# Optimization experiments

Hardware: AMD Instinct MI355X
Metric: run time of the kernel (lower is better)

## Reference

```python
import jax, jax.numpy as jnp
import numpy as np

IN, HID, RANK, B = 2048, 2048, 512, 8192


def setup_inputs() -> dict:
    key = jax.random.key(0)
    ks = jax.random.split(key, 16)
    s_in = 1.0 / np.sqrt(IN + HID)
    s_r = 1.0 / np.sqrt(RANK)
    inp = {
        "x": jax.random.normal(ks[0], (B, IN), jnp.float32),
        "h": jax.random.normal(ks[1], (B, HID), jnp.float32),
        "c": jax.random.normal(ks[2], (B, HID), jnp.float32),
    }
    names = ["i", "f", "c", "o"]
    for idx, g in enumerate(names):
        inp[f"U{g}"] = jax.random.uniform(ks[3 + 3 * idx], (IN + HID, RANK), jnp.float32, -s_in, s_in)
        inp[f"V{g}"] = jax.random.uniform(ks[4 + 3 * idx], (RANK, HID), jnp.float32, -s_r, s_r)
        inp[f"b{g}"] = jnp.zeros((HID,), jnp.float32)
    return inp


def reference(x, h, c, Ui, Vi, bi, Uf, Vf, bf, Uc, Vc, bc, Uo, Vo, bo):
    combined = jnp.concatenate([x, h], axis=1)  # [B, IN+HID]

    def gate(U, V, b):
        return (combined @ U) @ V + b  # low-rank: [B,R] then [B,HID]

    i = jax.nn.sigmoid(gate(Ui, Vi, bi))
    f = jax.nn.sigmoid(gate(Uf, Vf, bf))
    o = jax.nn.sigmoid(gate(Uo, Vo, bo))
    c_hat = jnp.tanh(gate(Uc, Vc, bc))
    c_new = f * c + i * c_hat
    h_new = o * jnp.tanh(c_new)
    return (h_new, c_new)
```

## Files before the change

### kernel.cpp

```cpp
#include <hip/hip_runtime.h>
#include <hip/hip_bf16.h>
#include <cstdint>
#include <cstddef>

typedef __bf16 bf16;
typedef __bf16 bf16x8 __attribute__((ext_vector_type(8)));
typedef float f32x4 __attribute__((ext_vector_type(4)));
typedef float f32x16 __attribute__((ext_vector_type(16)));

#define BATCH 8192
#define IN_DIM 2048
#define HID 2048
#define RANK 512
#define KDIM 4096
#define NG 2048


__device__ __forceinline__ void gload16(const void* g, void* l) {
  __builtin_amdgcn_global_load_lds(
      (const __attribute__((address_space(1))) unsigned int*)g,
      (__attribute__((address_space(3))) unsigned int*)l, 16, 0, 0);
}

__device__ __forceinline__ float sigmoidf_(float x) {
  return 1.0f / (1.0f + __expf(-x));
}
__device__ __forceinline__ float tanhf_(float x) {
  return 1.0f - 2.0f / (__expf(2.0f * x) + 1.0f);
}

#define GBAR  __builtin_amdgcn_s_barrier()
#define VMC2  asm volatile("s_waitcnt vmcnt(2)" ::: "memory")
#define VMC4  asm volatile("s_waitcnt vmcnt(4)" ::: "memory")
#define VMC8  asm volatile("s_waitcnt vmcnt(8)" ::: "memory")
#define SB0   __builtin_amdgcn_sched_barrier(0)
#define LGKMC(N) do { asm volatile("s_waitcnt lgkmcnt(" #N ")" ::: "memory"); SB0; } while (0)

__device__ __forceinline__ void stage_half(const bf16* __restrict__ g0, int ld,
                                           int row0, int kcol, bf16* lbase, int tid) {
  const int wid = tid >> 6;
  #pragma unroll
  for (int q = 0; q < 2; ++q) {
    const int slot = q * 512 + tid;
    const int row = slot >> 3, cb = slot & 7;
    const int gcb = cb ^ (row & 7);
    gload16(g0 + (size_t)(row0 + row) * ld + kcol + gcb * 8,
            lbase + (size_t)(q * 64 + wid * 8) * 64);
  }
}

__device__ __forceinline__ void stage_half32(const bf16* __restrict__ g0, int ld,
                                             int row0, int kcol, bf16* lbase, int tid) {
  const int wid = tid >> 6;
  #pragma unroll
  for (int q = 0; q < 2; ++q) {
    const int slot = q * 512 + tid;
    const int row = slot >> 3, cb = slot & 7;
    const int gcb = cb ^ (row & 7) ^ ((row >> 3) & 3);
    gload16(g0 + (size_t)(row0 + row) * ld + kcol + gcb * 8,
            lbase + (size_t)(q * 64 + wid * 8) * 64);
  }
}


#define LD_A32(PA, Q, P)                                                       \
  _Pragma("unroll") for (int s = 0; s < 4; ++s)                                \
    a[P][s] = *(const bf16x8*)((PA) + (wm + (Q) * 32 + c32) * 64               \
                               + (((2 * s + ko) ^ swz) << 3));

#define LD_B32(PB)                                                             \
  _Pragma("unroll") for (int ct = 0; ct < 2; ++ct)                             \
  _Pragma("unroll") for (int s = 0; s < 4; ++s)                                \
    b[ct][s] = *(const bf16x8*)((PB) + (wn + ct * 32 + c32) * 64               \
                                + (((2 * s + ko) ^ swz) << 3));

#define MFMA32(Q, P)                                                           \
  _Pragma("unroll") for (int s = 0; s < 4; ++s)                                \
  _Pragma("unroll") for (int ct = 0; ct < 2; ++ct)                             \
    acc[(Q) * 2 + ct] = __builtin_amdgcn_mfma_f32_32x32x16_bf16(               \
        a[P][s], b[ct][s], acc[(Q) * 2 + ct], 0, 0, 0);

template <int NT>
__device__ __forceinline__ void gemm_core32(const bf16* __restrict__ A, int lda, int m0,
                                            const bf16* __restrict__ B, int ldb, int n0,
                                            bf16* lds, f32x16 (&acc)[8]) {
  const int tid = threadIdx.x;
  const int wid = tid >> 6, lane = tid & 63;
  const int wm = (wid >> 2) * 128, wn = (wid & 3) * 64;
  const int c32 = lane & 31, ko = lane >> 5;
  const int swz = (c32 & 7) ^ ((c32 >> 3) & 3);
  bf16x8 a[2][4];
  bf16x8 b[2][4];

  bf16* Ab0 = lds;
  bf16* Ab1 = lds + 16384;
  bf16* Rg0 = lds + 2 * 16384;
  bf16* Rg1 = lds + 3 * 16384;
  bf16* Rg2 = lds + 4 * 16384;

  #pragma unroll
  for (int i = 0; i < 8; ++i)
    #pragma unroll
    for (int r = 0; r < 16; ++r) acc[i][r] = 0.f;

  stage_half32(A, lda, m0,       0,   Ab0,        tid);
  stage_half32(A, lda, m0 + 128, 0,   Ab0 + 8192, tid);
  stage_half32(B, ldb, n0,       0,   Rg0,        tid);
  stage_half32(B, ldb, n0 + 128, 0,   Rg0 + 8192, tid);
  stage_half32(B, ldb, n0,       64,  Rg1,        tid);
  stage_half32(B, ldb, n0 + 128, 64,  Rg1 + 8192, tid);
  stage_half32(B, ldb, n0,       128, Rg2,        tid);
  stage_half32(B, ldb, n0 + 128, 128, Rg2 + 8192, tid);
  VMC8;
  GBAR;
  LD_B32(Rg0);
  SB0;

  bf16 *pBc = Rg0, *pBn = Rg1, *pBn2 = Rg2;
  bf16 *pAc = Ab0, *pAa = Ab1;
  for (int c = 0; c < NT; ++c) {
    const int kc1 = ((c + 1) & (NT - 1)) * 64;
    const int kc3 = ((c + 3) & (NT - 1)) * 64;
    LD_A32(pAc, 0, 0); LD_A32(pAc, 1, 1); SB0;
    stage_half32(A, lda, m0,       kc1, pAa,        tid); SB0;
    GBAR;
    LGKMC(4);
    __builtin_amdgcn_s_setprio(1); MFMA32(0, 0); __builtin_amdgcn_s_setprio(0);
    LD_A32(pAc, 2, 0); SB0;
    stage_half32(A, lda, m0 + 128, kc1, pAa + 8192, tid); SB0;
    GBAR;
    LGKMC(4);
    __builtin_amdgcn_s_setprio(1); MFMA32(1, 1); __builtin_amdgcn_s_setprio(0);
    LD_A32(pAc, 3, 1); SB0;
    stage_half32(B, ldb, n0,       kc3, pBc,        tid); SB0;
    GBAR;
    LGKMC(4);
    __builtin_amdgcn_s_setprio(1); MFMA32(2, 0); __builtin_amdgcn_s_setprio(0);
    stage_half32(B, ldb, n0 + 128, kc3, pBc + 8192, tid); SB0;
    VMC4;
    GBAR;
    LGKMC(0);
    __builtin_amdgcn_s_setprio(1); MFMA32(3, 1); __builtin_amdgcn_s_setprio(0);
    LD_B32(pBn);
    SB0;
    bf16* tt = pBc; pBc = pBn; pBn = pBn2; pBn2 = tt;
    tt = pAc; pAc = pAa; pAa = tt;
  }
}


#define LD_Bp(PB)                                                              \
  _Pragma("unroll") for (int j = 0; j < 4; ++j)                                \
  _Pragma("unroll") for (int ks = 0; ks < 2; ++ks)                             \
    b[j][ks] = *(const bf16x8*)((PB) + (wn + j * 16 + lr) * 64                 \
                                 + ((((ks << 2) | lk) ^ sw) << 3));

#define LD_AP(PA, Q, P)                                                        \
  _Pragma("unroll") for (int ks = 0; ks < 2; ++ks)                             \
    ap[P][ks] = *(const bf16x8*)((PA) + (wm + (Q) * 16 + lr) * 64              \
                                 + ((((ks << 2) | lk) ^ sw) << 3));

#define MFMAP2(ACC, Q, P)                                                      \
  _Pragma("unroll") for (int ks = 0; ks < 2; ++ks)                             \
  _Pragma("unroll") for (int j = 0; j < 4; ++j)                                \
    ACC[(Q)][j] = __builtin_amdgcn_mfma_f32_16x16x32_bf16(                     \
        ap[P][ks], b[j][ks], ACC[(Q)][j], 0, 0, 0);

#define STEP2(ACC, ACOL, BPTR, BCOL)                                           \
  {                                                                            \
    LD_AP(pAc, 0, 0); LD_AP(pAc, 1, 1); SB0;                                   \
    stage_half(Rb, lda, m0,       (ACOL), pAa,        tid); SB0;               \
    GBAR;                                                                      \
    LGKMC(2);                                                                  \
    __builtin_amdgcn_s_setprio(1); MFMAP2(ACC, 0, 0); __builtin_amdgcn_s_setprio(0); \
    LD_AP(pAc, 2, 0); SB0;                                                     \
    stage_half(Rb, lda, m0 + 128, (ACOL), pAa + 8192, tid); SB0;               \
    GBAR;                                                                      \
    LGKMC(2);                                                                  \
    __builtin_amdgcn_s_setprio(1); MFMAP2(ACC, 1, 1); __builtin_amdgcn_s_setprio(0); \
    LD_AP(pAc, 3, 1); SB0;                                                     \
    stage_half((BPTR), ldb, n0, (BCOL), pBc, tid); SB0;                        \
    GBAR;                                                                      \
    LGKMC(2);                                                                  \
    __builtin_amdgcn_s_setprio(1); MFMAP2(ACC, 2, 0); __builtin_amdgcn_s_setprio(0); \
    VMC2;                                                                      \
    LGKMC(0);                                                                  \
    GBAR;                                                                      \
    __builtin_amdgcn_s_setprio(1); MFMAP2(ACC, 3, 1); __builtin_amdgcn_s_setprio(0); \
    LD_Bp(pBn);                                                                \
    SB0;                                                                       \
    bf16* tt_ = pBc; pBc = pBn; pBn = pBn2; pBn2 = tt_;                        \
    tt_ = pAc; pAc = pAa; pAa = tt_;                                           \
  }

template <int NT>
__device__ __forceinline__ void gemm_coreP2(
    const bf16* __restrict__ Rb, int lda, int m0, int kgA, int kgB,
    const bf16* __restrict__ VA, const bf16* __restrict__ VB, int ldb, int n0,
    bf16* lds, f32x4 (&accA)[4][4], f32x4 (&accB)[4][4]) {
  const int tid = threadIdx.x;
  const int wid = tid >> 6, lane = tid & 63;
  const int wm = (wid >> 1) * 64, wn = (wid & 1) * 64;
  const int lr = lane & 15, lk = lane >> 4;
  const int sw = lr & 7;
  bf16x8 ap[2][2], b[4][2];

  bf16* Ab0 = lds;
  bf16* Ab1 = lds + 16384;
  bf16* Rg0 = lds + 32768;
  bf16* Rg1 = lds + 40960;
  bf16* Rg2 = lds + 49152;

  #pragma unroll
  for (int i = 0; i < 4; ++i)
    #pragma unroll
    for (int j = 0; j < 4; ++j) {
      accA[i][j] = (f32x4){0.f, 0.f, 0.f, 0.f};
      accB[i][j] = (f32x4){0.f, 0.f, 0.f, 0.f};
    }

  stage_half(Rb, lda, m0,       kgA, Ab0,        tid);
  stage_half(Rb, lda, m0 + 128, kgA, Ab0 + 8192, tid);
  stage_half(VA, ldb, n0, 0,  Rg0, tid);
  stage_half(VB, ldb, n0, 0,  Rg1, tid);
  stage_half(VA, ldb, n0, 64, Rg2, tid);
  VMC4;
  GBAR;
  LD_Bp(Rg0);
  SB0;

  bf16 *pBc = Rg0, *pBn = Rg1, *pBn2 = Rg2;
  bf16 *pAc = Ab0, *pAa = Ab1;
  for (int t = 0; t < NT; ++t) {
    STEP2(accA, kgB + t * 64, VB, ((t + 1) & (NT - 1)) * 64);
    STEP2(accB, kgA + ((t + 1) & (NT - 1)) * 64, VA, ((t + 2) & (NT - 1)) * 64);
  }
}


__global__ void k_convert_combined(const float* __restrict__ x,
                                   const float* __restrict__ h,
                                   bf16* __restrict__ out) {
  size_t i4 = (size_t)blockIdx.x * blockDim.x + threadIdx.x;
  size_t base = i4 * 4;
  int col = (int)(base & (KDIM - 1));
  size_t row = base >> 12;
  const float* src = (col < IN_DIM) ? (x + row * IN_DIM + col)
                                    : (h + row * (size_t)HID + (col - IN_DIM));
  float4 v = *(const float4*)src;
  union { bf16 b[4]; uint2 u; } p;
  p.b[0] = (bf16)v.x; p.b[1] = (bf16)v.y; p.b[2] = (bf16)v.z; p.b[3] = (bf16)v.w;
  *(uint2*)(out + base) = p.u;
}


__global__ void k_tconv4v(const float* __restrict__ s0, const float* __restrict__ s1,
                          const float* __restrict__ s2, const float* __restrict__ s3,
                          bf16* __restrict__ out, int nrow, int ncol,
                          long ostride, long gstride) {
  __shared__ float t[64][65];
  const float* in = blockIdx.z == 0 ? s0 : blockIdx.z == 1 ? s1
                  : blockIdx.z == 2 ? s2 : s3;
  bf16* o = out + (size_t)blockIdx.z * gstride;
  const int c0 = blockIdx.x * 64, r0 = blockIdx.y * 64;
  const int tid = threadIdx.x;

  {
    const int rb = tid >> 4;
    const int cq = (tid & 15) * 4;
    #pragma unroll
    for (int i = 0; i < 4; ++i) {
      const int rr = rb + i * 16;
      float4 v = *(const float4*)(in + (size_t)(r0 + rr) * ncol + c0 + cq);
      t[rr][cq] = v.x; t[rr][cq + 1] = v.y; t[rr][cq + 2] = v.z; t[rr][cq + 3] = v.w;
    }
  }
  __syncthreads();
  {
    const int orow = tid >> 2;
    const int cb = (tid & 3) * 16;
    union { bf16 hh[8]; uint4 u; } p0, p1;
    #pragma unroll
    for (int k = 0; k < 8; ++k) p0.hh[k] = (bf16)t[cb + k][orow];
    #pragma unroll
    for (int k = 0; k < 8; ++k) p1.hh[k] = (bf16)t[cb + 8 + k][orow];
    bf16* ob = o + (size_t)(c0 + orow) * ostride + r0 + cb;
    *(uint4*)ob = p0.u;
    *(uint4*)(ob + 8) = p1.u;
  }
}


__launch_bounds__(512, 2)
__global__ void k_gemm1(const bf16* __restrict__ A,
                        const bf16* __restrict__ Bt,
                        bf16* __restrict__ R) {
  __shared__ __align__(16) bf16 lds[81920];
  const int bx = blockIdx.x;
  const int id = (bx & 7) * 32 + (bx >> 3);
  const int m0 = (id >> 3) * 256, n0 = (id & 7) * 256;
  f32x16 acc[8];
  gemm_core32<KDIM / 64>(A, KDIM, m0, Bt, KDIM, n0, lds, acc);

  const int tid = threadIdx.x;
  const int wid = tid >> 6, lane = tid & 63;
  const int wm = (wid >> 2) * 128, wn = (wid & 3) * 64;
  const int c32 = lane & 31, ko = lane >> 5;
  #pragma unroll
  for (int tix = 0; tix < 8; ++tix) {
    const int q = tix >> 1, ct = tix & 1;
    const int col = n0 + wn + ct * 32 + c32;
    const int rb = m0 + wm + q * 32 + 4 * ko;
    #pragma unroll
    for (int r = 0; r < 16; ++r) {
      const int row = rb + (r & 3) + 8 * (r >> 2);
      R[(size_t)row * NG + col] = (bf16)acc[tix][r];
    }
  }
}


__launch_bounds__(512, 2)
__global__ void k_pair_ic(const bf16* __restrict__ Rb,
                          const bf16* __restrict__ Vt,
                          const float* __restrict__ bi, const float* __restrict__ bc,
                          bf16* __restrict__ sv) {
  __shared__ __align__(16) bf16 lds[57344];
  const int bx = blockIdx.x;
  const int id = (bx & 7) * 64 + (bx >> 3);
  const int m0 = (id >> 4) * 256, n0 = (id & 15) * 128;

  f32x4 accI[4][4], accC[4][4];
  gemm_coreP2<RANK / 64>(Rb, NG, m0, 0 * RANK, 2 * RANK,
                         Vt + (size_t)0 * HID * RANK, Vt + (size_t)2 * HID * RANK,
                         RANK, n0, lds, accI, accC);

  const int tid = threadIdx.x;
  const int wid = tid >> 6, lane = tid & 63;
  const int wm = (wid >> 1) * 64, wn = (wid & 1) * 64;
  const int lr = lane & 15, lk = lane >> 4;
  #pragma unroll
  for (int j = 0; j < 4; ++j) {
    const int col = n0 + wn + j * 16 + lr;
    const float bji = bi[col], bjc = bc[col];
    #pragma unroll
    for (int q = 0; q < 4; ++q)
      #pragma unroll
      for (int v = 0; v < 4; ++v) {
        const int row = m0 + wm + q * 16 + lk * 4 + v;
        const float s = sigmoidf_(accI[q][j][v] + bji) * tanhf_(accC[q][j][v] + bjc);
        sv[(size_t)row * HID + col] = (bf16)s;
      }
  }
}


__launch_bounds__(512, 2)
__global__ void k_pair_fo(const bf16* __restrict__ Rb,
                          const bf16* __restrict__ Vt,
                          const float* __restrict__ bf_, const float* __restrict__ bo,
                          const bf16* __restrict__ sv,
                          const float* __restrict__ cin,
                          float* __restrict__ hout, float* __restrict__ cout) {
  __shared__ __align__(16) bf16 lds[57344];
  const int bx = blockIdx.x;
  const int id = (bx & 7) * 64 + (bx >> 3);
  const int m0 = (id >> 4) * 256, n0 = (id & 15) * 128;

  f32x4 accF[4][4], accO[4][4];
  gemm_coreP2<RANK / 64>(Rb, NG, m0, 1 * RANK, 3 * RANK,
                         Vt + (size_t)1 * HID * RANK, Vt + (size_t)3 * HID * RANK,
                         RANK, n0, lds, accF, accO);

  const int tid = threadIdx.x;
  const int wid = tid >> 6, lane = tid & 63;
  const int wm = (wid >> 1) * 64, wn = (wid & 1) * 64;
  const int lr = lane & 15, lk = lane >> 4;
  #pragma unroll
  for (int j = 0; j < 4; ++j) {
    const int col = n0 + wn + j * 16 + lr;
    const float bjf = bf_[col], bjo = bo[col];
    #pragma unroll
    for (int q = 0; q < 4; ++q)
      #pragma unroll
      for (int v = 0; v < 4; ++v) {
        const int row = m0 + wm + q * 16 + lk * 4 + v;
        const size_t e = (size_t)row * HID + col;
        const float f = sigmoidf_(accF[q][j][v] + bjf);
        const float cn = f * cin[e] + (float)sv[e];
        cout[e] = cn;
        hout[e] = sigmoidf_(accO[q][j][v] + bjo) * tanhf_(cn);
      }
  }
}


extern "C" void kernel_launch(void* const* d_in, const int* in_sizes, int n_in,
                              void* d_out, int out_size, void* d_ws, size_t ws_size,
                              hipStream_t stream) {
  const float* x = (const float*)d_in[0];
  const float* h = (const float*)d_in[1];
  const float* c = (const float*)d_in[2];
  const float* U[4] = {(const float*)d_in[3], (const float*)d_in[6],
                       (const float*)d_in[9], (const float*)d_in[12]};
  const float* V[4] = {(const float*)d_in[4], (const float*)d_in[7],
                       (const float*)d_in[10], (const float*)d_in[13]};
  const float* b[4] = {(const float*)d_in[5], (const float*)d_in[8],
                       (const float*)d_in[11], (const float*)d_in[14]};

  char* ws = (char*)d_ws;
  bf16* combined = (bf16*)ws;
  bf16* Ut       = (bf16*)(ws + 67108864);
  bf16* Vt       = (bf16*)(ws + 67108864 + 16777216);
  bf16* Rbuf     = (bf16*)(ws + 67108864 + 16777216 + 8388608);
  bf16* sv       = (bf16*)ws;

  float* hout = (float*)d_out;
  float* cout = hout + (size_t)BATCH * HID;

  k_convert_combined<<<(BATCH * (size_t)KDIM / 4) / 256, 256, 0, stream>>>(x, h, combined);

  k_tconv4v<<<dim3(RANK / 64, KDIM / 64, 4), 256, 0, stream>>>(
      U[0], U[1], U[2], U[3], Ut, KDIM, RANK, KDIM, (long)RANK * KDIM);
  k_tconv4v<<<dim3(HID / 64, RANK / 64, 4), 256, 0, stream>>>(
      V[0], V[1], V[2], V[3], Vt, RANK, HID, RANK, (long)HID * RANK);

  k_gemm1<<<256, 512, 0, stream>>>(combined, Ut, Rbuf);

  k_pair_ic<<<512, 512, 0, stream>>>(Rbuf, Vt, b[0], b[2], sv);
  k_pair_fo<<<512, 512, 0, stream>>>(Rbuf, Vt, b[1], b[3], sv, c, hout, cout);
}
```

Before: 328.5 us.

## Triple-buffer A tiles in low-rank gate GEMM pipeline

Adds a third LDS buffer for the A (rank-projection) tiles and prefetches both gates' first A tiles in the prologue, rotating three A buffers per step. The per-step global-load wait is relaxed from vmcnt(2) to vmcnt(6) so that more loads stay in flight while MFMAs run. This raises LDS use per block, which may constrain occupancy.

```diff
diff --git a/kernel.cpp b/kernel.cpp
--- a/kernel.cpp
+++ b/kernel.cpp
@@ -30,8 +30,8 @@
 }
 
 #define GBAR  __builtin_amdgcn_s_barrier()
-#define VMC2  asm volatile("s_waitcnt vmcnt(2)" ::: "memory")
 #define VMC4  asm volatile("s_waitcnt vmcnt(4)" ::: "memory")
+#define VMC6  asm volatile("s_waitcnt vmcnt(6)" ::: "memory")
 #define VMC8  asm volatile("s_waitcnt vmcnt(8)" ::: "memory")
 #define SB0   __builtin_amdgcn_sched_barrier(0)
 #define LGKMC(N) do { asm volatile("s_waitcnt lgkmcnt(" #N ")" ::: "memory"); SB0; } while (0)
@@ -166,35 +166,35 @@
     ACC[(Q)][j] = __builtin_amdgcn_mfma_f32_16x16x32_bf16(                     \
         ap[P][ks], b[j][ks], ACC[(Q)][j], 0, 0, 0);
 
-#define STEP2(ACC, ACOL, BPTR, BCOL)                                           \
+#define STEP3(ACC, ACOL, BPTR, BCOL)                                           \
   {                                                                            \
-    LD_AP(pAc, 0, 0); LD_AP(pAc, 1, 1); SB0;                                   \
-    stage_half(Rb, lda, m0,       (ACOL), pAa,        tid); SB0;               \
+    LD_AP(pA0, 0, 0); LD_AP(pA0, 1, 1); SB0;                                   \
+    stage_half(Rb, lda, m0,       (ACOL), pA2,        tid); SB0;               \
     GBAR;                                                                      \
     LGKMC(2);                                                                  \
     __builtin_amdgcn_s_setprio(1); MFMAP2(ACC, 0, 0); __builtin_amdgcn_s_setprio(0); \
-    LD_AP(pAc, 2, 0); SB0;                                                     \
-    stage_half(Rb, lda, m0 + 128, (ACOL), pAa + 8192, tid); SB0;               \
+    LD_AP(pA0, 2, 0); SB0;                                                     \
+    stage_half(Rb, lda, m0 + 128, (ACOL), pA2 + 8192, tid); SB0;               \
     GBAR;                                                                      \
     LGKMC(2);                                                                  \
     __builtin_amdgcn_s_setprio(1); MFMAP2(ACC, 1, 1); __builtin_amdgcn_s_setprio(0); \
-    LD_AP(pAc, 3, 1); SB0;                                                     \
+    LD_AP(pA0, 3, 1); SB0;                                                     \
     stage_half((BPTR), ldb, n0, (BCOL), pBc, tid); SB0;                        \
     GBAR;                                                                      \
     LGKMC(2);                                                                  \
     __builtin_amdgcn_s_setprio(1); MFMAP2(ACC, 2, 0); __builtin_amdgcn_s_setprio(0); \
-    VMC2;                                                                      \
+    VMC6;                                                                      \
     LGKMC(0);                                                                  \
     GBAR;                                                                      \
     __builtin_amdgcn_s_setprio(1); MFMAP2(ACC, 3, 1); __builtin_amdgcn_s_setprio(0); \
     LD_Bp(pBn);                                                                \
     SB0;                                                                       \
     bf16* tt_ = pBc; pBc = pBn; pBn = pBn2; pBn2 = tt_;                        \
-    tt_ = pAc; pAc = pAa; pAa = tt_;                                           \
+    tt_ = pA0; pA0 = pA1; pA1 = pA2; pA2 = tt_;                                \
   }
 
 template <int NT>
-__device__ __forceinline__ void gemm_coreP2(
+__device__ __forceinline__ void gemm_coreP3(
     const bf16* __restrict__ Rb, int lda, int m0, int kgA, int kgB,
     const bf16* __restrict__ VA, const bf16* __restrict__ VB, int ldb, int n0,
     bf16* lds, f32x4 (&accA)[4][4], f32x4 (&accB)[4][4]) {
@@ -207,9 +207,10 @@
 
   bf16* Ab0 = lds;
   bf16* Ab1 = lds + 16384;
-  bf16* Rg0 = lds + 32768;
-  bf16* Rg1 = lds + 40960;
-  bf16* Rg2 = lds + 49152;
+  bf16* Ab2 = lds + 32768;
+  bf16* Rg0 = lds + 49152;
+  bf16* Rg1 = lds + 57344;
+  bf16* Rg2 = lds + 65536;
 
   #pragma unroll
   for (int i = 0; i < 4; ++i)
@@ -222,18 +223,20 @@
   stage_half(Rb, lda, m0,       kgA, Ab0,        tid);
   stage_half(Rb, lda, m0 + 128, kgA, Ab0 + 8192, tid);
   stage_half(VA, ldb, n0, 0,  Rg0, tid);
+  stage_half(Rb, lda, m0,       kgB, Ab1,        tid);
+  stage_half(Rb, lda, m0 + 128, kgB, Ab1 + 8192, tid);
   stage_half(VB, ldb, n0, 0,  Rg1, tid);
   stage_half(VA, ldb, n0, 64, Rg2, tid);
-  VMC4;
+  VMC8;
   GBAR;
   LD_Bp(Rg0);
   SB0;
 
   bf16 *pBc = Rg0, *pBn = Rg1, *pBn2 = Rg2;
-  bf16 *pAc = Ab0, *pAa = Ab1;
+  bf16 *pA0 = Ab0, *pA1 = Ab1, *pA2 = Ab2;
   for (int t = 0; t < NT; ++t) {
-    STEP2(accA, kgB + t * 64, VB, ((t + 1) & (NT - 1)) * 64);
-    STEP2(accB, kgA + ((t + 1) & (NT - 1)) * 64, VA, ((t + 2) & (NT - 1)) * 64);
+    STEP3(accA, kgA + ((t + 1) & (NT - 1)) * 64, VB, ((t + 1) & (NT - 1)) * 64);
+    STEP3(accB, kgB + ((t + 1) & (NT - 1)) * 64, VA, ((t + 2) & (NT - 1)) * 64);
   }
 }
 
@@ -325,13 +328,13 @@
                           const bf16* __restrict__ Vt,
                           const float* __restrict__ bi, const float* __restrict__ bc,
                           bf16* __restrict__ sv) {
-  __shared__ __align__(16) bf16 lds[57344];
+  __shared__ __align__(16) bf16 lds[73728];
   const int bx = blockIdx.x;
   const int id = (bx & 7) * 64 + (bx >> 3);
   const int m0 = (id >> 4) * 256, n0 = (id & 15) * 128;
 
   f32x4 accI[4][4], accC[4][4];
-  gemm_coreP2<RANK / 64>(Rb, NG, m0, 0 * RANK, 2 * RANK,
+  gemm_coreP3<RANK / 64>(Rb, NG, m0, 0 * RANK, 2 * RANK,
                          Vt + (size_t)0 * HID * RANK, Vt + (size_t)2 * HID * RANK,
                          RANK, n0, lds, accI, accC);
 
@@ -362,13 +365,13 @@
                           const bf16* __restrict__ sv,
                           const float* __restrict__ cin,
                           float* __restrict__ hout, float* __restrict__ cout) {
-  __shared__ __align__(16) bf16 lds[57344];
+  __shared__ __align__(16) bf16 lds[73728];
   const int bx = blockIdx.x;
   const int id = (bx & 7) * 64 + (bx >> 3);
   const int m0 = (id >> 4) * 256, n0 = (id & 15) * 128;
 
   f32x4 accF[4][4], accO[4][4];
-  gemm_coreP2<RANK / 64>(Rb, NG, m0, 1 * RANK, 3 * RANK,
+  gemm_coreP3<RANK / 64>(Rb, NG, m0, 1 * RANK, 3 * RANK,
                          Vt + (size_t)1 * HID * RANK, Vt + (size_t)3 * HID * RANK,
                          RANK, n0, lds, accF, accO);
 
```

Result: no change. 326.5 us (-0.6%).
